# Kernel tuning notes

Measured on AMD Instinct MI355X. Metric: run time of the kernel, lower is better.

Reference implementation:

```python
import jax, jax.numpy as jnp
import numpy as np

N_NODES = 50000
N_EDGES = 800000
HIDDEN = 128
N_REL = 64
NUM_HEADS = 8
HEAD_DIM = HIDDEN // NUM_HEADS


def setup_inputs() -> dict:
    key = jax.random.key(0)
    ks = jax.random.split(key, 20)
    s = 0.05
    inp = {
        "x": jax.random.normal(ks[0], (N_NODES, HIDDEN), dtype=jnp.float32),
        "timestamps": jax.random.uniform(ks[1], (N_NODES,), dtype=jnp.float32),
        "src": jax.random.randint(ks[2], (N_EDGES,), 0, N_NODES),
        "dst": jax.random.randint(ks[3], (N_EDGES,), 0, N_NODES),
        "edge_type": jax.random.randint(ks[4], (N_EDGES,), 0, N_REL),
        "edge_time": jax.random.uniform(ks[5], (N_EDGES,), dtype=jnp.float32),
        # parameters (torch Linear stored as [in, out] so we use x @ W + b)
        "rel_table": jax.random.normal(ks[6], (N_REL, HIDDEN), dtype=jnp.float32) * s,
        "Wq": jax.random.normal(ks[7], (HIDDEN, HIDDEN), dtype=jnp.float32) * s,
        "bq": jnp.zeros((HIDDEN,), dtype=jnp.float32),
        "Wk": jax.random.normal(ks[8], (HIDDEN, HIDDEN), dtype=jnp.float32) * s,
        "bk": jnp.zeros((HIDDEN,), dtype=jnp.float32),
        "Wv": jax.random.normal(ks[9], (HIDDEN, HIDDEN), dtype=jnp.float32) * s,
        "bv": jnp.zeros((HIDDEN,), dtype=jnp.float32),
        "W1": jax.random.normal(ks[10], (2 * HIDDEN + 1, HIDDEN), dtype=jnp.float32) * s,
        "b1": jnp.zeros((HIDDEN,), dtype=jnp.float32),
        "W2": jax.random.normal(ks[11], (HIDDEN, 1), dtype=jnp.float32) * s,
        "b2": jnp.zeros((1,), dtype=jnp.float32),
        "time_coeff": jnp.array(1.0, dtype=jnp.float32),
    }
    return inp


def reference(x, timestamps, src, dst, edge_type, edge_time, rel_table,
              Wq, bq, Wk, bk, Wv, bv, W1, b1, W2, b2, time_coeff):
    N = x.shape[0]
    # temporal gating
    delta_t = (timestamps[dst] - edge_time) / (jnp.abs(time_coeff) + 1e-9)  # [E]
    time_mask = jax.nn.sigmoid(delta_t)[:, None]                            # [E,1]
    rel_emb = rel_table[edge_type] * time_mask                              # [E,H]
    src_emb = x[src]                                                        # [E,H]
    # dynamic edge weights: MLP([src_emb, rel_emb, time_mask]) -> sigmoid
    weight_input = jnp.concatenate([src_emb, rel_emb, time_mask], axis=-1)  # [E,2H+1]
    h = jax.nn.relu(weight_input @ W1 + b1)
    dynamic_weights = jax.nn.sigmoid(h @ W2 + b2)                           # [E,1]
    message = src_emb * rel_emb * dynamic_weights                           # [E,H]
    # multi-head edge attention keyed by dst
    q = (x[dst] @ Wq + bq).reshape(-1, NUM_HEADS, HEAD_DIM)
    k = (message @ Wk + bk).reshape(-1, NUM_HEADS, HEAD_DIM)
    v = (message @ Wv + bv).reshape(-1, NUM_HEADS, HEAD_DIM)
    scores = (q * k).sum(-1) / (HEAD_DIM ** 0.5)                            # [E,heads]
    # scatter softmax over edges grouped by dst
    seg_max = jax.ops.segment_max(scores, dst, num_segments=N)              # [N,heads]
    e = jnp.exp(scores - seg_max[dst])
    denom = jax.ops.segment_sum(e, dst, num_segments=N)
    attn = e / denom[dst]                                                   # [E,heads]
    out = jax.ops.segment_sum(v * attn[..., None], dst, num_segments=N)     # [N,heads,hd]
    return out.reshape(N, NUM_HEADS * HEAD_DIM)
```

## Files before the change

kernel.cpp:

```cpp
#include <hip/hip_runtime.h>

typedef __bf16 v8bf __attribute__((ext_vector_type(8)));
typedef __bf16 v4bf __attribute__((ext_vector_type(4)));
typedef float  v4f  __attribute__((ext_vector_type(4)));

#define MFMA16x16x32 __builtin_amdgcn_mfma_f32_16x16x32_bf16

#define HIDDEN 128
#define NHEADS 8

__global__ __launch_bounds__(256) void prep_hist(
    const float* __restrict__ rel, const float* __restrict__ W1,
    const float* __restrict__ Wk, const float* __restrict__ Wv,
    const float* __restrict__ W2, const int* __restrict__ dst,
    int* __restrict__ count,
    __bf16* __restrict__ mlppre, __bf16* __restrict__ relbf,
    __bf16* __restrict__ wswz, __bf16* __restrict__ w2bf,
    float* __restrict__ outz, int E, int hb, int nz4)
{
  const int b = blockIdx.x;
  if (b < 64) {
    __shared__ float rrow[128];
    const int j = threadIdx.x;
    if (j < 128) rrow[j] = rel[b*HIDDEN + j];
    __syncthreads();
    if (j < 128) {
      float acc = W1[256*HIDDEN + j];
      #pragma unroll 4
      for (int k=0;k<128;k++) acc += rrow[k]*W1[(128+k)*HIDDEN + j];
      mlppre[b*HIDDEN + j] = (__bf16)acc;
      relbf [b*HIDDEN + j] = (__bf16)rrow[j];
    }
  } else if (b < 80) {
    int f = (b - 64)*256 + threadIdx.x;
    if (f < 128) w2bf[f] = (__bf16)W2[f];
    if (f >= 2*8*4*64) return;
    int lane = f & 63, kk = (f>>6)&3, c = (f>>8)&7, mat = f>>11;
    const float* W = mat ? Wv : Wk;
    int qq = lane>>4, nn = lane&15;
    v8bf o;
    #pragma unroll
    for (int j=0;j<8;j++) o[j] = (__bf16)W[(kk*32 + qq*8 + j)*HIDDEN + c*16 + nn];
    *(v8bf*)(wswz + (long)f*8) = o;
  } else if (b < 80 + hb) {
    long i = (long)(b - 80)*256 + threadIdx.x;
    long e4 = i*4;
    if (e4 + 3 < E) {
      int4 d = *(const int4*)(dst + e4);
      atomicAdd(&count[d.x], 1);
      atomicAdd(&count[d.y], 1);
      atomicAdd(&count[d.z], 1);
      atomicAdd(&count[d.w], 1);
    } else {
      for (long e = e4; e < E; e++) atomicAdd(&count[dst[e]], 1);
    }
  } else {
    int idx = (b - 80 - hb)*256 + threadIdx.x;
    if (idx < nz4) ((float4*)outz)[idx] = make_float4(0.f,0.f,0.f,0.f);
  }
}

__global__ __launch_bounds__(1024) void scan_kernel(const int* __restrict__ count,
    int* __restrict__ base, int N)
{
  __shared__ int ssum[1024];
  const int t = threadIdx.x;
  const int chunk = ((N + 4095) >> 12) << 2;
  const int lo = t*chunk, hi = min(lo + chunk, N);
  int s = 0;
  int i = lo;
  for (; i + 3 < hi; i += 4) {
    int4 v = *(const int4*)(count + i);
    s += v.x + v.y + v.z + v.w;
  }
  for (; i < hi; i++) s += count[i];
  ssum[t] = s;
  __syncthreads();
  #pragma unroll
  for (int ofs = 1; ofs < 1024; ofs <<= 1) {
    int v = (t >= ofs) ? ssum[t - ofs] : 0;
    __syncthreads();
    ssum[t] += v;
    __syncthreads();
  }
  int run = (t == 0) ? 0 : ssum[t-1];
  i = lo;
  for (; i + 3 < hi; i += 4) {
    int4 c = *(const int4*)(count + i);
    int4 o;
    o.x = run; o.y = run + c.x; o.z = o.y + c.y; o.w = o.z + c.z;
    *(int4*)(base + i) = o;
    run = o.w + c.w;
  }
  for (; i < hi; i++) { base[i] = run; run += count[i]; }
}

__global__ __launch_bounds__(512) void scat_pre(
    const float* __restrict__ x, const float* __restrict__ Wq,
    const float* __restrict__ bq, const float* __restrict__ W1,
    const float* __restrict__ b1,
    const int* __restrict__ src, const int* __restrict__ dstp,
    const int* __restrict__ etyp, const float* __restrict__ etime,
    const float* __restrict__ ts, const float* __restrict__ tc,
    const int* __restrict__ base, int* __restrict__ cursor,
    int4* __restrict__ meta4,
    __bf16* __restrict__ qbf, __bf16* __restrict__ hpre, __bf16* __restrict__ xbf,
    int N, int E, int SB)
{
  __shared__ __bf16 X[32][136];
  if ((int)blockIdx.x < SB) {
    int e = blockIdx.x*512 + threadIdx.x;
    if (e < E) {
      int d = dstp[e];
      int pI = base[d] + atomicAdd(&cursor[d], 1);
      float invtc = 1.0f / (fabsf(tc[0]) + 1e-9f);
      float dt = (ts[d] - etime[e]) * invtc;
      float tm = 1.0f/(1.0f + __expf(-dt));
      meta4[pI] = make_int4(src[e], d, etyp[e], __float_as_int(tm));
    }
    return;
  }
  const int pb = blockIdx.x - SB, npb = gridDim.x - SB;
  const int tid = threadIdx.x;
  const int w = tid >> 6, l = tid & 63, qd = l >> 4, ln = l & 15;
  const int col = w*16 + ln;

  v8bf BQ[4], BH[4];
  #pragma unroll
  for (int kk=0; kk<4; kk++) {
    v8bf f, g;
    #pragma unroll
    for (int j=0;j<8;j++){
      f[j] = (__bf16)Wq[(kk*32 + qd*8 + j)*HIDDEN + col];
      g[j] = (__bf16)W1[(kk*32 + qd*8 + j)*HIDDEN + col];
    }
    BQ[kk] = f; BH[kk] = g;
  }
  const float bqv = bq[col], b1v = b1[col];

  const int s = tid >> 4, c8 = (tid & 15)*8;
  for (int n0 = pb*32; n0 < N; n0 += npb*32) {
    __syncthreads();
    int n = n0 + s;
    v8bf xv;
    if (n < N) {
      const float4* xp = (const float4*)(x + (long)n*HIDDEN + c8);
      float4 a = xp[0], b = xp[1];
      xv[0]=(__bf16)a.x; xv[1]=(__bf16)a.y; xv[2]=(__bf16)a.z; xv[3]=(__bf16)a.w;
      xv[4]=(__bf16)b.x; xv[5]=(__bf16)b.y; xv[6]=(__bf16)b.z; xv[7]=(__bf16)b.w;
      *(v8bf*)(xbf + (long)n*HIDDEN + c8) = xv;
    } else {
      #pragma unroll
      for (int j=0;j<8;j++) xv[j] = (__bf16)0.f;
    }
    *(v8bf*)&X[s][c8] = xv;
    __syncthreads();

    v4f q0={0.f,0.f,0.f,0.f}, q1={0.f,0.f,0.f,0.f};
    v4f h0={0.f,0.f,0.f,0.f}, h1={0.f,0.f,0.f,0.f};
    #pragma unroll
    for (int kk=0;kk<4;kk++) {
      v8bf a0 = *(const v8bf*)&X[ln][kk*32 + qd*8];
      v8bf a1 = *(const v8bf*)&X[16+ln][kk*32 + qd*8];
      q0 = MFMA16x16x32(a0, BQ[kk], q0, 0,0,0);
      q1 = MFMA16x16x32(a1, BQ[kk], q1, 0,0,0);
      h0 = MFMA16x16x32(a0, BH[kk], h0, 0,0,0);
      h1 = MFMA16x16x32(a1, BH[kk], h1, 0,0,0);
    }
    #pragma unroll
    for (int r=0;r<4;r++) {
      int n_o = n0 + qd*4 + r;
      if (n_o < N) {
        qbf [(long)n_o*HIDDEN + col] = (__bf16)(q0[r] + bqv);
        hpre[(long)n_o*HIDDEN + col] = (__bf16)(h0[r] + b1v);
      }
      int n2 = n0 + 16 + qd*4 + r;
      if (n2 < N) {
        qbf [(long)n2*HIDDEN + col] = (__bf16)(q1[r] + bqv);
        hpre[(long)n2*HIDDEN + col] = (__bf16)(h1[r] + b1v);
      }
    }
  }
}

__global__ __launch_bounds__(512, 4) void edge_fused4(
    const int4* __restrict__ meta4, const float* __restrict__ b2,
    const __bf16* __restrict__ xbf, const __bf16* __restrict__ hpre,
    const __bf16* __restrict__ qbf, const __bf16* __restrict__ relbf,
    const __bf16* __restrict__ mlppre, const __bf16* __restrict__ w2bf,
    const __bf16* __restrict__ wswz,
    const float* __restrict__ bk, const float* __restrict__ bv,
    float* __restrict__ out, float* __restrict__ denom, int E, int ntiles)
{
  __shared__ __align__(16) __bf16 MSG[2][4096];

  const int tid = threadIdx.x;
  const int wid = tid >> 6, l = tid & 63, qd = l >> 4, ln = l & 15;
  const int eIdx = wid*4 + (l >> 4);
  const int lc = l & 15;

  v8bf bkf[4], bvf[4];
  #pragma unroll
  for (int kk=0;kk<4;kk++){
    bkf[kk] = *(const v8bf*)(wswz +         wid*2048 + kk*512 + (size_t)l*8);
    bvf[kk] = *(const v8bf*)(wswz + 16384 + wid*2048 + kk*512 + (size_t)l*8);
  }
  const float bkc = bk[wid*16 + ln];
  const float bvc = bv[wid*16 + ln];
  const float b2v = b2[0];
  const v8bf w2v = *(const v8bf*)(w2bf + lc*8);

  const int g = gridDim.x;
  int t = blockIdx.x;
  if (t >= ntiles) return;

  int4 mt = make_int4(0, -1, 0, 0);
  { int e = t*32 + l; if (l < 32 && e < E) mt = meta4[e]; }
  int tn = t + g;
  int4 mtn = make_int4(0, -1, 0, 0);
  if (tn < ntiles) { int e = tn*32 + l; if (l < 32 && e < E) mtn = meta4[e]; }

  float tmE = __int_as_float(__shfl(mt.w, eIdx));
  v8bf sv, av, rv, bp;
  {
    int srcE = __shfl(mt.x, eIdx);
    int tyE  = __shfl(mt.z, eIdx);
    sv = *(const v8bf*)(xbf   + (long)srcE*HIDDEN + lc*8);
    av = *(const v8bf*)(hpre  + (long)srcE*HIDDEN + lc*8);
    rv = *(const v8bf*)(relbf + (long)tyE *HIDDEN + lc*8);
    bp = *(const v8bf*)(mlppre+ (long)tyE *HIDDEN + lc*8);
  }

  int p = 0;
  while (true) {
    const int d_m = mt.y;

    int dprev = __shfl(d_m, (l>0)?(l-1):0);
    int flag = (l < 32) && ((l==0) || (d_m != dprev));
    unsigned long long segmask = __ballot(flag);

    int dC[2][4];
    #pragma unroll
    for (int b=0;b<2;b++)
      #pragma unroll
      for (int r=0;r<4;r++) dC[b][r] = __shfl(d_m, b*16 + qd*4 + r);

    const int t2 = tn + g;
    int4 mt2 = make_int4(0, -1, 0, 0);
    if (t2 < ntiles) { int e = t2*32 + l; if (l < 32 && e < E) mt2 = meta4[e]; }

    const float tmN = __int_as_float(__shfl(mtn.w, eIdx));
    const int srcN = __shfl(mtn.x, eIdx);
    const int tyN  = __shfl(mtn.z, eIdx);

    float z = 0.f;
    #pragma unroll
    for (int j=0;j<8;j++){
      float pj = (float)av[j] + tmE*(float)bp[j];
      z += fmaxf(pj, 0.f)*(float)w2v[j];
    }
    z += __shfl_xor(z,1); z += __shfl_xor(z,2);
    z += __shfl_xor(z,4); z += __shfl_xor(z,8);
    const float dw = 1.0f/(1.0f + __expf(-(z + b2v)));
    const float sM = tmE * dw;

    {
      char* wbase = (char*)&MSG[p][0] + eIdx*256;
      const int sw = (eIdx & 7) << 4;
      v8bf m;
      #pragma unroll
      for (int j=0;j<8;j++) m[j] = (__bf16)((float)sv[j]*(float)rv[j]*sM);
      *(v8bf*)(wbase + ((lc*16) ^ sw)) = m;
    }

    sv = *(const v8bf*)(xbf   + (long)srcN*HIDDEN + lc*8);
    av = *(const v8bf*)(hpre  + (long)srcN*HIDDEN + lc*8);
    rv = *(const v8bf*)(relbf + (long)tyN *HIDDEN + lc*8);
    bp = *(const v8bf*)(mlppre+ (long)tyN *HIDDEN + lc*8);

    asm volatile("s_waitcnt lgkmcnt(0)" ::: "memory");
    __builtin_amdgcn_s_barrier();

    float qv[2][4];
    #pragma unroll
    for (int b=0;b<2;b++)
      #pragma unroll
      for (int r=0;r<4;r++){
        int d = dC[b][r];
        qv[b][r] = (float)qbf[(long)(d<0?0:d)*HIDDEN + wid*16 + ln];
      }

    const char* rb = (const char*)&MSG[p][0];
    v4f aK[2], aV[2];
    __builtin_amdgcn_s_setprio(1);
    #pragma unroll
    for (int b=0;b<2;b++){
      const int rrow = b*16 + ln;
      const char* abase = rb + rrow*256;
      const int asw = (rrow & 7) << 4;
      v4f k_ = {0.f,0.f,0.f,0.f}, v_ = {0.f,0.f,0.f,0.f};
      #pragma unroll
      for (int kk=0;kk<4;kk++){
        v8bf a = *(const v8bf*)(abase + ((kk*64 + qd*16) ^ asw));
        k_ = MFMA16x16x32(a, bkf[kk], k_, 0,0,0);
        v_ = MFMA16x16x32(a, bvf[kk], v_, 0,0,0);
      }
      aK[b] = k_; aV[b] = v_;
    }
    __builtin_amdgcn_s_setprio(0);

    float sc[2][4];
    #pragma unroll
    for (int b=0;b<2;b++)
      #pragma unroll
      for (int r=0;r<4;r++) sc[b][r] = (aK[b][r] + bkc)*qv[b][r];
    #pragma unroll
    for (int m=1;m<16;m<<=1){
      #pragma unroll
      for (int b=0;b<2;b++)
        #pragma unroll
        for (int r=0;r<4;r++) sc[b][r] += __shfl_xor(sc[b][r], m);
    }
    float ee[2][4], wv[2][4];
    #pragma unroll
    for (int b=0;b<2;b++)
      #pragma unroll
      for (int r=0;r<4;r++){
        float e_ = __expf(sc[b][r]*0.25f);
        ee[b][r] = e_;
        wv[b][r] = e_*(aV[b][r] + bvc);
      }

    unsigned long long mm = segmask;
    while (mm){
      int s0 = __ffsll((long long)mm) - 1;
      mm &= mm - 1;
      int s1 = mm ? (__ffsll((long long)mm) - 1) : 32;
      int dseg = __shfl(d_m, s0);
      if (dseg < 0) continue;
      float a0 = 0.f, dn0 = 0.f;
      #pragma unroll
      for (int b=0;b<2;b++)
        #pragma unroll
        for (int r=0;r<4;r++){
          int rw = b*16 + qd*4 + r;
          bool in = (rw >= s0) && (rw < s1);
          a0  += in ? wv[b][r] : 0.f;
          dn0 += in ? ee[b][r] : 0.f;
        }
      a0  += __shfl_xor(a0,16);  a0  += __shfl_xor(a0,32);
      dn0 += __shfl_xor(dn0,16); dn0 += __shfl_xor(dn0,32);
      if (l < 16) atomicAdd(&out[(long)dseg*HIDDEN + wid*16 + ln], a0);
      if (l == 0) atomicAdd(&denom[(long)dseg*NHEADS + wid], dn0);
    }

    if (tn >= ntiles) break;
    t = tn; tn = t2; mt = mtn; mtn = mt2; tmE = tmN;
    p ^= 1;
  }
}

__global__ __launch_bounds__(512) void q_kernel(const float* __restrict__ x,
    const float* __restrict__ Wq, const float* __restrict__ bq,
    float* __restrict__ q, int N)
{
  __shared__ __bf16 X[32][136];
  const int tid = threadIdx.x;
  const int w = tid >> 6, l = tid & 63, qd = l >> 4, ln = l & 15;
  const int col = w*16 + ln;
  v8bf B[4];
  #pragma unroll
  for (int kk=0; kk<4; kk++) {
    v8bf f;
    #pragma unroll
    for (int j=0;j<8;j++) f[j] = (__bf16)Wq[(kk*32 + qd*8 + j)*HIDDEN + col];
    B[kk] = f;
  }
  const float bqv = bq[col];
  const int s = tid >> 4, c8 = (tid & 15)*8;
  for (int n0 = blockIdx.x*32; n0 < N; n0 += gridDim.x*32) {
    __syncthreads();
    int n = n0 + s;
    v8bf xv;
    if (n < N) {
      const float4* xp = (const float4*)(x + (long)n*HIDDEN + c8);
      float4 a = xp[0], b = xp[1];
      xv[0]=(__bf16)a.x; xv[1]=(__bf16)a.y; xv[2]=(__bf16)a.z; xv[3]=(__bf16)a.w;
      xv[4]=(__bf16)b.x; xv[5]=(__bf16)b.y; xv[6]=(__bf16)b.z; xv[7]=(__bf16)b.w;
    } else {
      #pragma unroll
      for (int j=0;j<8;j++) xv[j] = (__bf16)0.f;
    }
    *(v8bf*)&X[s][c8] = xv;
    __syncthreads();
    v4f acc0 = {0.f,0.f,0.f,0.f}, acc1 = {0.f,0.f,0.f,0.f};
    #pragma unroll
    for (int kk=0;kk<4;kk++) {
      v8bf a0 = *(const v8bf*)&X[ln][kk*32 + qd*8];
      v8bf a1 = *(const v8bf*)&X[16+ln][kk*32 + qd*8];
      acc0 = MFMA16x16x32(a0, B[kk], acc0, 0,0,0);
      acc1 = MFMA16x16x32(a1, B[kk], acc1, 0,0,0);
    }
    #pragma unroll
    for (int r=0;r<4;r++) {
      int n_o = n0 + qd*4 + r;
      if (n_o < N) q[(long)n_o*HIDDEN + col] = acc0[r] + bqv;
      int n_o2 = n0 + 16 + qd*4 + r;
      if (n_o2 < N) q[(long)n_o2*HIDDEN + col] = acc1[r] + bqv;
    }
  }
}

__global__ __launch_bounds__(512) void edge_atomic(
    const float* __restrict__ x, const float* __restrict__ ts,
    const int* __restrict__ src, const int* __restrict__ dst,
    const int* __restrict__ etyp, const float* __restrict__ etime,
    const float* __restrict__ rel,
    const float* __restrict__ Wk, const float* __restrict__ bk,
    const float* __restrict__ Wv, const float* __restrict__ bv,
    const float* __restrict__ W1, const float* __restrict__ b1,
    const float* __restrict__ W2, const float* __restrict__ b2,
    const float* __restrict__ tc,
    const float* __restrict__ qws, float* __restrict__ denom,
    float* __restrict__ out, int E)
{
  __shared__ __bf16 A[32][264];
  __shared__ __bf16 A2[32][136];
  __shared__ float sW2[128], sb1[128], sw1r[128], sbk[128], sbv[128];
  __shared__ float stm[32], sdw[32];
  __shared__ int   ssrc[32], sdst[32], styp[32];
  __shared__ float dwpart[8][32];
  const int tid = threadIdx.x;
  const int w = tid >> 6, l = tid & 63, qd = l >> 4, ln = l & 15;
  const int col = w*16 + ln;
  v8bf B1[8], BK[4], BV[4];
  #pragma unroll
  for (int kk=0;kk<8;kk++){ v8bf f;
    #pragma unroll
    for (int j=0;j<8;j++) f[j] = (__bf16)W1[(kk*32+qd*8+j)*HIDDEN + col];
    B1[kk]=f; }
  #pragma unroll
  for (int kk=0;kk<4;kk++){ v8bf f,g;
    #pragma unroll
    for (int j=0;j<8;j++){ f[j] = (__bf16)Wk[(kk*32+qd*8+j)*HIDDEN + col];
                           g[j] = (__bf16)Wv[(kk*32+qd*8+j)*HIDDEN + col]; }
    BK[kk]=f; BV[kk]=g; }
  if (tid < 128) {
    sW2[tid]=W2[tid]; sb1[tid]=b1[tid]; sw1r[tid]=W1[256*HIDDEN+tid];
    sbk[tid]=bk[tid]; sbv[tid]=bv[tid];
  }
  const float b2v = b2[0];
  const float invtc = 1.0f / (fabsf(tc[0]) + 1e-9f);
  const int s = tid >> 4, c8 = (tid & 15)*8;
  const int ntiles = (E + 31) >> 5;
  for (int t = blockIdx.x; t < ntiles; t += gridDim.x) {
    const int e0 = t*32;
    __syncthreads();
    if (tid < 32) {
      int e = e0 + tid;
      if (e < E) {
        int d = dst[e];
        ssrc[tid]=src[e]; sdst[tid]=d; styp[tid]=etyp[e];
        float dt = (ts[d] - etime[e]) * invtc;
        stm[tid] = 1.0f/(1.0f+expf(-dt));
      } else { ssrc[tid]=0; sdst[tid]=0; styp[tid]=0; stm[tid]=0.f; }
    }
    __syncthreads();
    {
      const float tmv = stm[s];
      const float4* xp = (const float4*)(x + (long)ssrc[s]*HIDDEN + c8);
      float4 a = xp[0], b = xp[1];
      const float4* rp = (const float4*)(rel + (long)styp[s]*HIDDEN + c8);
      float4 ra = rp[0], rb = rp[1];
      v8bf sv, rv;
      sv[0]=(__bf16)a.x; sv[1]=(__bf16)a.y; sv[2]=(__bf16)a.z; sv[3]=(__bf16)a.w;
      sv[4]=(__bf16)b.x; sv[5]=(__bf16)b.y; sv[6]=(__bf16)b.z; sv[7]=(__bf16)b.w;
      rv[0]=(__bf16)(ra.x*tmv); rv[1]=(__bf16)(ra.y*tmv);
      rv[2]=(__bf16)(ra.z*tmv); rv[3]=(__bf16)(ra.w*tmv);
      rv[4]=(__bf16)(rb.x*tmv); rv[5]=(__bf16)(rb.y*tmv);
      rv[6]=(__bf16)(rb.z*tmv); rv[7]=(__bf16)(rb.w*tmv);
      *(v8bf*)&A[s][c8] = sv;
      *(v8bf*)&A[s][128 + c8] = rv;
    }
    __syncthreads();
    v4f acc0={0.f,0.f,0.f,0.f}, acc1={0.f,0.f,0.f,0.f};
    #pragma unroll
    for (int kk=0;kk<8;kk++){
      v8bf a0 = *(const v8bf*)&A[ln][kk*32 + qd*8];
      v8bf a1 = *(const v8bf*)&A[16+ln][kk*32 + qd*8];
      acc0 = MFMA16x16x32(a0, B1[kk], acc0, 0,0,0);
      acc1 = MFMA16x16x32(a1, B1[kk], acc1, 0,0,0);
    }
    float part[8];
    {
      const float w1rj = sw1r[col], b1j = sb1[col], w2j = sW2[col];
      #pragma unroll
      for (int r=0;r<4;r++){
        int i0 = qd*4 + r, i1 = 16 + qd*4 + r;
        part[r]   = fmaxf(acc0[r] + stm[i0]*w1rj + b1j, 0.f)*w2j;
        part[4+r] = fmaxf(acc1[r] + stm[i1]*w1rj + b1j, 0.f)*w2j;
      }
    }
    #pragma unroll
    for (int m=1;m<16;m<<=1){
      #pragma unroll
      for (int i=0;i<8;i++) part[i] += __shfl_xor(part[i], m, 16);
    }
    if (ln == 0){
      #pragma unroll
      for (int r=0;r<4;r++){ dwpart[w][qd*4+r]=part[r]; dwpart[w][16+qd*4+r]=part[4+r]; }
    }
    __syncthreads();
    if (tid < 32){
      float z = b2v;
      #pragma unroll
      for (int ww=0;ww<8;ww++) z += dwpart[ww][tid];
      sdw[tid] = 1.0f/(1.0f+expf(-z));
    }
    __syncthreads();
    {
      const float dwv = sdw[s];
      v8bf mv;
      #pragma unroll
      for (int i=0;i<8;i++)
        mv[i] = (__bf16)((float)A[s][c8+i]*(float)A[s][128+c8+i]*dwv);
      *(v8bf*)&A2[s][c8] = mv;
    }
    __syncthreads();
    v4f k0={0.f,0.f,0.f,0.f}, k1={0.f,0.f,0.f,0.f};
    v4f v0={0.f,0.f,0.f,0.f}, v1={0.f,0.f,0.f,0.f};
    #pragma unroll
    for (int kk=0;kk<4;kk++){
      v8bf a0 = *(const v8bf*)&A2[ln][kk*32 + qd*8];
      v8bf a1 = *(const v8bf*)&A2[16+ln][kk*32 + qd*8];
      k0 = MFMA16x16x32(a0, BK[kk], k0, 0,0,0);
      k1 = MFMA16x16x32(a1, BK[kk], k1, 0,0,0);
      v0 = MFMA16x16x32(a0, BV[kk], v0, 0,0,0);
      v1 = MFMA16x16x32(a1, BV[kk], v1, 0,0,0);
    }
    float sc[8];
    const float bkj = sbk[col], bvj = sbv[col];
    #pragma unroll
    for (int r=0;r<4;r++){
      int i0 = qd*4 + r, i1 = 16 + qd*4 + r;
      sc[r]   = (k0[r]+bkj)*qws[(long)sdst[i0]*HIDDEN + col];
      sc[4+r] = (k1[r]+bkj)*qws[(long)sdst[i1]*HIDDEN + col];
    }
    #pragma unroll
    for (int m=1;m<16;m<<=1){
      #pragma unroll
      for (int i=0;i<8;i++) sc[i] += __shfl_xor(sc[i], m, 16);
    }
    float ee[8];
    #pragma unroll
    for (int i=0;i<8;i++) ee[i] = expf(sc[i]*0.25f);
    if (ln == 0){
      #pragma unroll
      for (int r=0;r<4;r++){
        int i0 = qd*4 + r, i1 = 16 + qd*4 + r;
        if (e0+i0 < E) atomicAdd(&denom[(long)sdst[i0]*NHEADS + w], ee[r]);
        if (e0+i1 < E) atomicAdd(&denom[(long)sdst[i1]*NHEADS + w], ee[4+r]);
      }
    }
    #pragma unroll
    for (int r=0;r<4;r++){
      int i0 = qd*4 + r, i1 = 16 + qd*4 + r;
      if (e0+i0 < E) atomicAdd(&out[(long)sdst[i0]*HIDDEN + col], ee[r]*(v0[r]+bvj));
      if (e0+i1 < E) atomicAdd(&out[(long)sdst[i1]*HIDDEN + col], ee[4+r]*(v1[r]+bvj));
    }
  }
}

__global__ void fin_kernel(float* __restrict__ out, const float* __restrict__ denom, int N)
{
  int idx = blockIdx.x*blockDim.x + threadIdx.x;
  int total = N*32;
  if (idx < total){
    int n = idx >> 5;
    int h = (idx & 31) >> 2;
    float d = denom[n*8 + h];
    float inv = d > 0.f ? 1.0f/d : 0.f;
    float4* p = (float4*)out + idx;
    float4 v = *p;
    v.x*=inv; v.y*=inv; v.z*=inv; v.w*=inv;
    *p = v;
  }
}

static inline size_t align256(size_t v){ return (v + 255) & ~(size_t)255; }

extern "C" void kernel_launch(void* const* d_in, const int* in_sizes, int n_in,
                              void* d_out, int out_size, void* d_ws, size_t ws_size,
                              hipStream_t stream)
{
  const float* x      = (const float*)d_in[0];
  const float* ts     = (const float*)d_in[1];
  const int*   src    = (const int*)d_in[2];
  const int*   dstp   = (const int*)d_in[3];
  const int*   etyp   = (const int*)d_in[4];
  const float* etime  = (const float*)d_in[5];
  const float* rel    = (const float*)d_in[6];
  const float* Wq     = (const float*)d_in[7];
  const float* bq     = (const float*)d_in[8];
  const float* Wk     = (const float*)d_in[9];
  const float* bk     = (const float*)d_in[10];
  const float* Wv     = (const float*)d_in[11];
  const float* bv     = (const float*)d_in[12];
  const float* W1     = (const float*)d_in[13];
  const float* b1     = (const float*)d_in[14];
  const float* W2     = (const float*)d_in[15];
  const float* b2     = (const float*)d_in[16];
  const float* tc     = (const float*)d_in[17];
  float* out = (float*)d_out;

  const int N = in_sizes[0] / HIDDEN;
  const int E = in_sizes[2];

  char* ws = (char*)d_ws;
  size_t off = 0;
  __bf16* qbf    = (__bf16*)(ws + off); off += align256((size_t)N*HIDDEN*2);
  __bf16* hpre   = (__bf16*)(ws + off); off += align256((size_t)N*HIDDEN*2);
  __bf16* xbf    = (__bf16*)(ws + off); off += align256((size_t)N*HIDDEN*2);
  __bf16* relbf  = (__bf16*)(ws + off); off += align256((size_t)64*HIDDEN*2);
  __bf16* mlppre = (__bf16*)(ws + off); off += align256((size_t)64*HIDDEN*2);
  __bf16* w2bf   = (__bf16*)(ws + off); off += align256((size_t)HIDDEN*2);
  __bf16* wswz   = (__bf16*)(ws + off); off += align256((size_t)4096*8*2);
  size_t zoff = off;
  int*    countp = (int*)(ws + off);    off += align256((size_t)N*4);
  int*    cursor = (int*)(ws + off);    off += align256((size_t)N*4);
  float*  denom  = (float*)(ws + off);  off += align256((size_t)N*NHEADS*4);
  size_t zlen = off - zoff;
  int4*   meta4  = (int4*)(ws + off);   off += align256((size_t)E*16);
  int*    basep  = (int*)(ws + off);    off += align256((size_t)N*4);
  const size_t needed_fast = off;

  if (ws_size >= needed_fast) {
    hipMemsetAsync(ws + zoff, 0, zlen, stream);

    const int hb = (E + 1023)/1024;
    const int nz4 = N*32;
    const int zb = (nz4 + 255)/256;
    prep_hist<<<80 + hb + zb, 256, 0, stream>>>(rel, W1, Wk, Wv, W2, dstp, countp,
        mlppre, relbf, wswz, w2bf, out, E, hb, nz4);
    scan_kernel<<<1, 1024, 0, stream>>>(countp, basep, N);
    const int SB = (E + 511)/512;
    scat_pre<<<SB + 1024, 512, 0, stream>>>(x, Wq, bq, W1, b1,
        src, dstp, etyp, etime, ts, tc, basep, cursor, meta4,
        qbf, hpre, xbf, N, E, SB);

    const int ntiles = (E + 31) >> 5;
    edge_fused4<<<1024, 512, 0, stream>>>(meta4, b2,
        xbf, hpre, qbf, relbf, mlppre, w2bf, wswz, bk, bv, out, denom, E, ntiles);
    fin_kernel<<<(N*32 + 255)/256, 256, 0, stream>>>(out, denom, N);
  } else {
    float* qws    = (float*)ws;
    float* denom2 = (float*)(ws + align256((size_t)N*HIDDEN*4));
    hipMemsetAsync(out,    0, (size_t)N*HIDDEN*4, stream);
    hipMemsetAsync(denom2, 0, (size_t)N*NHEADS*4, stream);
    q_kernel<<<512, 512, 0, stream>>>(x, Wq, bq, qws, N);
    edge_atomic<<<512, 512, 0, stream>>>(x, ts, src, dstp, etyp, etime, rel,
        Wk, bk, Wv, bv, W1, b1, W2, b2, tc, qws, denom2, out, E);
    fin_kernel<<<(N*32 + 255)/256, 256, 0, stream>>>(out, denom2, N);
  }
}
```

Baseline: 505.8 us.

## Split dynamic-weight MLP into separate kernel and prefetch q one tile ahead

The per-edge dynamic-weight computation (hpre/mlppre gather, ReLU dot with W2, sigmoid) moves into a new dw_kernel that writes time_mask*dw back into the meta4 time slot. The main edge kernel no longer gathers hpre and mlppre rows, so its register use and gather traffic go down. The q gathers for the next tile are now issued before the barrier and carried over, hiding their latency behind the current tile's MFMA work. In exchange there is an extra kernel launch plus an extra pass that reads meta4 and the two bf16 row gathers, and more registers are held live for the prefetched q values.

```diff
diff --git a/kernel.cpp b/kernel.cpp
--- a/kernel.cpp
+++ b/kernel.cpp
@@ -183,12 +183,48 @@
   }
 }
 
-__global__ __launch_bounds__(512, 4) void edge_fused4(
-    const int4* __restrict__ meta4, const float* __restrict__ b2,
-    const __bf16* __restrict__ xbf, const __bf16* __restrict__ hpre,
-    const __bf16* __restrict__ qbf, const __bf16* __restrict__ relbf,
-    const __bf16* __restrict__ mlppre, const __bf16* __restrict__ w2bf,
-    const __bf16* __restrict__ wswz,
+__global__ __launch_bounds__(256) void dw_kernel(
+    int4* __restrict__ meta4,
+    const __bf16* __restrict__ hpre, const __bf16* __restrict__ mlppre,
+    const __bf16* __restrict__ w2bf, const float* __restrict__ b2, int E)
+{
+  const int tid = threadIdx.x;
+  const int wid = tid >> 6, l = tid & 63;
+  const int e0 = (blockIdx.x*4 + wid)*4;
+  const int ei = l >> 4, lc = l & 15;
+
+  int4 mt = make_int4(0, -1, 0, 0);
+  if (l < 4 && e0 + l < E) mt = meta4[e0 + l];
+  const int srcE = __shfl(mt.x, ei);
+  const int tyE  = __shfl(mt.z, ei);
+  const float tm = __int_as_float(__shfl(mt.w, ei));
+
+  const v8bf w2v = *(const v8bf*)(w2bf + lc*8);
+  v8bf av = *(const v8bf*)(hpre  + (long)srcE*HIDDEN + lc*8);
+  v8bf bp = *(const v8bf*)(mlppre+ (long)tyE *HIDDEN + lc*8);
+
+  float z = 0.f;
+  #pragma unroll
+  for (int j=0;j<8;j++){
+    float pj = (float)av[j] + tm*(float)bp[j];
+    z += fmaxf(pj, 0.f)*(float)w2v[j];
+  }
+  z += __shfl_xor(z,1); z += __shfl_xor(z,2);
+  z += __shfl_xor(z,4); z += __shfl_xor(z,8);
+
+  if (lc == 0) {
+    int e = e0 + ei;
+    if (e < E) {
+      float dw = 1.0f/(1.0f + __expf(-(z + b2[0])));
+      ((int*)meta4)[(long)e*4 + 3] = __float_as_int(tm * dw);
+    }
+  }
+}
+
+__global__ __launch_bounds__(512, 4) void edge_fused5(
+    const int4* __restrict__ meta4,
+    const __bf16* __restrict__ xbf, const __bf16* __restrict__ qbf,
+    const __bf16* __restrict__ relbf, const __bf16* __restrict__ wswz,
     const float* __restrict__ bk, const float* __restrict__ bv,
     float* __restrict__ out, float* __restrict__ denom, int E, int ntiles)
 {
@@ -196,8 +232,7 @@
 
   const int tid = threadIdx.x;
   const int wid = tid >> 6, l = tid & 63, qd = l >> 4, ln = l & 15;
-  const int eIdx = wid*4 + (l >> 4);
-  const int lc = l & 15;
+  const int eIdx = wid*4 + qd;
 
   v8bf bkf[4], bvf[4];
   #pragma unroll
@@ -207,8 +242,6 @@
   }
   const float bkc = bk[wid*16 + ln];
   const float bvc = bv[wid*16 + ln];
-  const float b2v = b2[0];
-  const v8bf w2v = *(const v8bf*)(w2bf + lc*8);
 
   const int g = gridDim.x;
   int t = blockIdx.x;
@@ -220,16 +253,27 @@
   int4 mtn = make_int4(0, -1, 0, 0);
   if (tn < ntiles) { int e = tn*32 + l; if (l < 32 && e < E) mtn = meta4[e]; }
 
-  float tmE = __int_as_float(__shfl(mt.w, eIdx));
-  v8bf sv, av, rv, bp;
+  float sME = __int_as_float(__shfl(mt.w, eIdx));
+  v8bf sv, rv;
   {
     int srcE = __shfl(mt.x, eIdx);
     int tyE  = __shfl(mt.z, eIdx);
-    sv = *(const v8bf*)(xbf   + (long)srcE*HIDDEN + lc*8);
-    av = *(const v8bf*)(hpre  + (long)srcE*HIDDEN + lc*8);
-    rv = *(const v8bf*)(relbf + (long)tyE *HIDDEN + lc*8);
-    bp = *(const v8bf*)(mlppre+ (long)tyE *HIDDEN + lc*8);
-  }
+    sv = *(const v8bf*)(xbf   + (long)srcE*HIDDEN + ln*8);
+    rv = *(const v8bf*)(relbf + (long)tyE *HIDDEN + ln*8);
+  }
+  int dC[2][4];
+  #pragma unroll
+  for (int b=0;b<2;b++)
+    #pragma unroll
+    for (int r=0;r<4;r++) dC[b][r] = __shfl(mt.y, b*16 + qd*4 + r);
+  float qA[2][4];
+  #pragma unroll
+  for (int b=0;b<2;b++)
+    #pragma unroll
+    for (int r=0;r<4;r++){
+      int d = dC[b][r];
+      qA[b][r] = (float)qbf[(long)(d<0?0:d)*HIDDEN + wid*16 + ln];
+    }
 
   int p = 0;
   while (true) {
@@ -239,56 +283,43 @@
     int flag = (l < 32) && ((l==0) || (d_m != dprev));
     unsigned long long segmask = __ballot(flag);
 
-    int dC[2][4];
-    #pragma unroll
-    for (int b=0;b<2;b++)
-      #pragma unroll
-      for (int r=0;r<4;r++) dC[b][r] = __shfl(d_m, b*16 + qd*4 + r);
-
     const int t2 = tn + g;
     int4 mt2 = make_int4(0, -1, 0, 0);
     if (t2 < ntiles) { int e = t2*32 + l; if (l < 32 && e < E) mt2 = meta4[e]; }
 
-    const float tmN = __int_as_float(__shfl(mtn.w, eIdx));
+    const float sMN = __int_as_float(__shfl(mtn.w, eIdx));
     const int srcN = __shfl(mtn.x, eIdx);
     const int tyN  = __shfl(mtn.z, eIdx);
-
-    float z = 0.f;
-    #pragma unroll
-    for (int j=0;j<8;j++){
-      float pj = (float)av[j] + tmE*(float)bp[j];
-      z += fmaxf(pj, 0.f)*(float)w2v[j];
-    }
-    z += __shfl_xor(z,1); z += __shfl_xor(z,2);
-    z += __shfl_xor(z,4); z += __shfl_xor(z,8);
-    const float dw = 1.0f/(1.0f + __expf(-(z + b2v)));
-    const float sM = tmE * dw;
+    int dN[2][4];
+    #pragma unroll
+    for (int b=0;b<2;b++)
+      #pragma unroll
+      for (int r=0;r<4;r++) dN[b][r] = __shfl(mtn.y, b*16 + qd*4 + r);
 
     {
       char* wbase = (char*)&MSG[p][0] + eIdx*256;
       const int sw = (eIdx & 7) << 4;
       v8bf m;
       #pragma unroll
-      for (int j=0;j<8;j++) m[j] = (__bf16)((float)sv[j]*(float)rv[j]*sM);
-      *(v8bf*)(wbase + ((lc*16) ^ sw)) = m;
-    }
-
-    sv = *(const v8bf*)(xbf   + (long)srcN*HIDDEN + lc*8);
-    av = *(const v8bf*)(hpre  + (long)srcN*HIDDEN + lc*8);
-    rv = *(const v8bf*)(relbf + (long)tyN *HIDDEN + lc*8);
-    bp = *(const v8bf*)(mlppre+ (long)tyN *HIDDEN + lc*8);
+      for (int j=0;j<8;j++) m[j] = (__bf16)((float)sv[j]*(float)rv[j]*sME);
+      *(v8bf*)(wbase + ((ln*16) ^ sw)) = m;
+    }
+
+    sv = *(const v8bf*)(xbf   + (long)srcN*HIDDEN + ln*8);
+    rv = *(const v8bf*)(relbf + (long)tyN *HIDDEN + ln*8);
+
+    float qB[2][4];
+    #pragma unroll
+    for (int b=0;b<2;b++)
+      #pragma unroll
+      for (int r=0;r<4;r++){
+        int d = dN[b][r];
+        qB[b][r] = (float)qbf[(long)(d<0?0:d)*HIDDEN + wid*16 + ln];
+      }
 
     asm volatile("s_waitcnt lgkmcnt(0)" ::: "memory");
     __builtin_amdgcn_s_barrier();
-
-    float qv[2][4];
-    #pragma unroll
-    for (int b=0;b<2;b++)
-      #pragma unroll
-      for (int r=0;r<4;r++){
-        int d = dC[b][r];
-        qv[b][r] = (float)qbf[(long)(d<0?0:d)*HIDDEN + wid*16 + ln];
-      }
+    __builtin_amdgcn_sched_barrier(0);
 
     const char* rb = (const char*)&MSG[p][0];
     v4f aK[2], aV[2];
@@ -313,7 +344,7 @@
     #pragma unroll
     for (int b=0;b<2;b++)
       #pragma unroll
-      for (int r=0;r<4;r++) sc[b][r] = (aK[b][r] + bkc)*qv[b][r];
+      for (int r=0;r<4;r++) sc[b][r] = (aK[b][r] + bkc)*qA[b][r];
     #pragma unroll
     for (int m=1;m<16;m<<=1){
       #pragma unroll
@@ -355,7 +386,14 @@
     }
 
     if (tn >= ntiles) break;
-    t = tn; tn = t2; mt = mtn; mtn = mt2; tmE = tmN;
+    t = tn; tn = t2; mt = mtn; mtn = mt2; sME = sMN;
+    #pragma unroll
+    for (int b=0;b<2;b++)
+      #pragma unroll
+      for (int r=0;r<4;r++){
+        dC[b][r] = dN[b][r];
+        qA[b][r] = qB[b][r];
+      }
     p ^= 1;
   }
 }
@@ -647,10 +685,11 @@
     scat_pre<<<SB + 1024, 512, 0, stream>>>(x, Wq, bq, W1, b1,
         src, dstp, etyp, etime, ts, tc, basep, cursor, meta4,
         qbf, hpre, xbf, N, E, SB);
+    dw_kernel<<<(E + 15)/16, 256, 0, stream>>>(meta4, hpre, mlppre, w2bf, b2, E);
 
     const int ntiles = (E + 31) >> 5;
-    edge_fused4<<<1024, 512, 0, stream>>>(meta4, b2,
-        xbf, hpre, qbf, relbf, mlppre, w2bf, wswz, bk, bv, out, denom, E, ntiles);
+    edge_fused5<<<1024, 512, 0, stream>>>(meta4,
+        xbf, qbf, relbf, wswz, bk, bv, out, denom, E, ntiles);
     fin_kernel<<<(N*32 + 255)/256, 256, 0, stream>>>(out, denom, N);
   } else {
     float* qws    = (float*)ws;
```

New measurement: 480.4 us. 1.05x faster.
